# Kernel optimization log

Measured on AMD Instinct MI355X. Metric: run time of the kernel, lower is better.

Reference implementation:

```python
import jax, jax.numpy as jnp
import numpy as np

NH, NKV, D = 16, 8, 128
HID = 2048
EPS = 1e-6
ROPE_BASE = 10000.0
T = 2048


def setup_inputs() -> dict:
    key = jax.random.key(0)
    k1, k2, k3 = jax.random.split(key, 3)
    return {
        "positions": jnp.arange(T, dtype=jnp.int32),
        "hidden_states": jax.random.normal(k1, (T, HID), dtype=jnp.float32),
        "w_qkv": jax.random.normal(k2, (HID, (NH + 2 * NKV) * D), dtype=jnp.float32) * 0.02,
        "w_o": jax.random.normal(k3, (NH * D, HID), dtype=jnp.float32) * 0.02,
        "q_norm_w": jnp.ones((D,), dtype=jnp.float32),
        "k_norm_w": jnp.ones((D,), dtype=jnp.float32),
    }


def _rmsnorm(x, w):
    # per-head RMSNorm over last dim (head_dim)
    return x * jax.lax.rsqrt(jnp.mean(x * x, axis=-1, keepdims=True) + EPS) * w


def reference(positions, hidden_states, w_qkv, w_o, q_norm_w, k_norm_w):
    t = hidden_states.shape[0]
    scale = D ** -0.5

    # fused QKV projection, then split
    qkv = hidden_states @ w_qkv                       # [T, (NH+2*NKV)*D]
    q, k, v = jnp.split(qkv, [NH * D, (NH + NKV) * D], axis=-1)
    q = q.reshape(t, NH, D)
    k = k.reshape(t, NKV, D)
    v = v.reshape(t, NKV, D)

    # per-head QK RMSNorm (Qwen3)
    q = _rmsnorm(q, q_norm_w)
    k = _rmsnorm(k, k_norm_w)

    # RoPE (neox style: rotate half-split pairs)
    inv_freq = 1.0 / (ROPE_BASE ** (jnp.arange(0, D, 2, dtype=jnp.float32) / D))
    freqs = positions.astype(jnp.float32)[:, None] * inv_freq  # [T, D/2]
    cos = jnp.cos(freqs)[:, None, :]                   # [T, 1, D/2]
    sin = jnp.sin(freqs)[:, None, :]

    def rope(x):
        x1, x2 = jnp.split(x, 2, axis=-1)
        return jnp.concatenate([x1 * cos - x2 * sin, x2 * cos + x1 * sin], axis=-1)

    q = rope(q)
    k = rope(k)

    # GQA: repeat kv heads
    g = NH // NKV
    kr = jnp.repeat(k, g, axis=1)                      # [T, NH, D]
    vr = jnp.repeat(v, g, axis=1)

    # causal attention
    scores = jnp.einsum('thd,shd->hts', q, kr) * scale  # [NH, T, T]
    causal = jnp.tril(jnp.ones((t, t), dtype=bool))
    scores = jnp.where(causal[None], scores, -jnp.inf)
    probs = jax.nn.softmax(scores, axis=-1)
    o = jnp.einsum('hts,shd->thd', probs, vr).reshape(t, NH * D)

    return o @ w_o
```

## Files before the change

### kernel.cpp

```cpp
#include <hip/hip_runtime.h>
#include <math.h>

#define T_TOK 2048
#define HIDDEN 2048
#define NH 16
#define NKV 8
#define DH 128

typedef unsigned short u16;
typedef __attribute__((ext_vector_type(8))) short bf16x8;
typedef __attribute__((ext_vector_type(4))) float f32x4;

__device__ __forceinline__ u16 f2bf(float f) {
  union { float f; unsigned u; } x; x.f = f;
  unsigned r = (x.u + 0x7fffu + ((x.u >> 16) & 1u)) >> 16;
  return (u16)r;
}

__device__ __forceinline__ float bf2f(u16 v) {
  union { unsigned u; float f; } x; x.u = ((unsigned)v) << 16;
  return x.f;
}

__device__ __forceinline__ void gload16(const void* g, void* l) {
  __builtin_amdgcn_global_load_lds((const __attribute__((address_space(1))) void*)g,
                                   (__attribute__((address_space(3))) void*)l,
                                   16, 0, 0);
}

__global__ __launch_bounds__(256) void prepass(const float* __restrict__ hidden,
                                               const float* __restrict__ w_qkv,
                                               const float* __restrict__ w_o,
                                               u16* __restrict__ Xb,
                                               u16* __restrict__ WqkvT,
                                               u16* __restrict__ WoT) {
  __shared__ float tile[64][65];
  const int b = blockIdx.x;
  if (b < 4096) {
    int i = b * 256 + threadIdx.x;
    float4 v = ((const float4*)hidden)[i];
    ushort4 o;
    o.x = f2bf(v.x); o.y = f2bf(v.y); o.z = f2bf(v.z); o.w = f2bf(v.w);
    ((ushort4*)Xb)[i] = o;
    return;
  }
  const float* in; u16* out; int R, Cdim, c0, r0;
  if (b < 6144) {
    int bb = b - 4096;
    in = w_qkv; out = WqkvT; R = 2048; Cdim = 4096;
    c0 = (bb & 63) * 64; r0 = (bb >> 6) * 64;
  } else {
    int bb = b - 6144;
    in = w_o; out = WoT; R = 2048; Cdim = 2048;
    c0 = (bb & 31) * 64; r0 = (bb >> 5) * 64;
  }
  const int tx = threadIdx.x & 63, ty = threadIdx.x >> 6;
#pragma unroll
  for (int i = 0; i < 64; i += 4)
    tile[ty + i][tx] = in[(size_t)(r0 + ty + i) * Cdim + c0 + tx];
  __syncthreads();
#pragma unroll
  for (int i = 0; i < 64; i += 4)
    out[(size_t)(c0 + ty + i) * R + r0 + tx] = f2bf(tile[tx][ty + i]);
}

__global__ __launch_bounds__(256) void add_parts4(const u16* __restrict__ a,
                                                  const u16* __restrict__ b,
                                                  const u16* __restrict__ c,
                                                  const u16* __restrict__ d,
                                                  float* __restrict__ o, int n4) {
  int i = blockIdx.x * blockDim.x + threadIdx.x;
  if (i < n4) {
    ushort4 x = ((const ushort4*)a)[i], y = ((const ushort4*)b)[i];
    ushort4 u = ((const ushort4*)c)[i], v = ((const ushort4*)d)[i];
    float4 z;
    z.x = bf2f(x.x) + bf2f(y.x) + bf2f(u.x) + bf2f(v.x);
    z.y = bf2f(x.y) + bf2f(y.y) + bf2f(u.y) + bf2f(v.y);
    z.z = bf2f(x.z) + bf2f(y.z) + bf2f(u.z) + bf2f(v.z);
    z.w = bf2f(x.w) + bf2f(y.w) + bf2f(u.w) + bf2f(v.w);
    ((float4*)o)[i] = z;
  }
}

__global__ __launch_bounds__(256) void rope_vt(const u16* __restrict__ qkv0,
                                               const u16* __restrict__ qkv1,
                                               const int* __restrict__ pos,
                                               const float* __restrict__ qw,
                                               const float* __restrict__ kw,
                                               u16* __restrict__ Qg,
                                               u16* __restrict__ Kg,
                                               u16* __restrict__ Vt,
                                               unsigned* __restrict__ counter) {
  __shared__ float tile[64][65];
  const int b = blockIdx.x;
  if (b < 12288) {
    const int wave = threadIdx.x >> 6, j = threadIdx.x & 63;
    const int idx = b * 4 + wave;
    const int t = idx & 2047, slot = idx >> 11;
    const float QSC = 0.088388347648318447f * 1.4426950408889634f;
    const size_t base_i = (size_t)t * 4096 + slot * 128;
    float x1 = bf2f(qkv0[base_i + j]) + bf2f(qkv1[base_i + j]);
    float x2 = bf2f(qkv0[base_i + j + 64]) + bf2f(qkv1[base_i + j + 64]);
    float ss = x1 * x1 + x2 * x2;
#pragma unroll
    for (int m = 1; m < 64; m <<= 1) ss += __shfl_xor(ss, m);
    float r = rsqrtf(ss * (1.0f / 128.0f) + 1e-6f);
    const bool isq = slot < NH;
    const float* w = isq ? qw : kw;
    float xn1 = x1 * r * w[j], xn2 = x2 * r * w[j + 64];
    float fp = (float)pos[t];
    float inv_freq = exp2f(-(float)j * (13.287712379549449f / 64.0f));
    float ang = fp * inv_freq;
    float sn, cs;
    sincosf(ang, &sn, &cs);
    float o1 = xn1 * cs - xn2 * sn;
    float o2 = xn2 * cs + xn1 * sn;
    if (isq) {
      size_t base = ((size_t)slot * T_TOK + t) * DH;
      Qg[base + j] = f2bf(o1 * QSC); Qg[base + 64 + j] = f2bf(o2 * QSC);
    } else {
      size_t base = ((size_t)(slot - NH) * T_TOK + t) * DH;
      Kg[base + j] = f2bf(o1); Kg[base + 64 + j] = f2bf(o2);
    }
    return;
  }
  if (b == 12288 && threadIdx.x == 0) *counter = 0u;
  const int bb = b - 12288;
  const int h = bb & 7, rest = bb >> 3;
  const int t0 = (rest & 31) * 64, d0 = (rest >> 5) * 64;
  const int tx = threadIdx.x & 63, ty = threadIdx.x >> 6;
#pragma unroll
  for (int i = 0; i < 64; i += 4) {
    size_t gi = (size_t)(t0 + ty + i) * 4096 + (NH + NKV) * DH + h * DH + d0 + tx;
    tile[ty + i][tx] = bf2f(qkv0[gi]) + bf2f(qkv1[gi]);
  }
  __syncthreads();
#pragma unroll
  for (int i = 0; i < 64; i += 4)
    Vt[((size_t)h * DH + d0 + ty + i) * T_TOK + t0 + tx] = f2bf(tile[tx][ty + i]);
}

__global__ __launch_bounds__(256) void gemm_bf16(const u16* __restrict__ A,
                                                 const u16* __restrict__ Bt,
                                                 void* __restrict__ Cout,
                                                 int M, int N, int K, int lda, int ldb,
                                                 int obf16) {
  __shared__ u16 Alds[128 * 64];
  __shared__ u16 Blds[128 * 64];
  A += (size_t)blockIdx.z * K;
  Bt += (size_t)blockIdx.z * K;
  const int m0 = blockIdx.y * 128, n0 = blockIdx.x * 128;
  const int wave = threadIdx.x >> 6, lane = threadIdx.x & 63;
  const int l15 = lane & 15, quad = lane >> 4;
  const int wr = wave >> 1, wc = wave & 1;

  const f32x4 zero = {0.f, 0.f, 0.f, 0.f};
  f32x4 acc[4][4];
#pragma unroll
  for (int i = 0; i < 4; ++i)
#pragma unroll
    for (int j = 0; j < 4; ++j) acc[i][j] = zero;

  for (int k0 = 0; k0 < K; k0 += 64) {
    __syncthreads();
#pragma unroll
    for (int c = 0; c < 4; ++c) {
      int chunk = wave * 4 + c;
      int slot = chunk * 64 + lane;
      int row = slot >> 3;
      int g = (slot & 7) ^ (row & 7);
      gload16(A + (size_t)(m0 + row) * lda + k0 + g * 8, &Alds[chunk * 512]);
      gload16(Bt + (size_t)(n0 + row) * ldb + k0 + g * 8, &Blds[chunk * 512]);
    }
    __syncthreads();
#pragma unroll
    for (int ksub = 0; ksub < 2; ++ksub) {
      bf16x8 af[4], bfr[4];
#pragma unroll
      for (int mt = 0; mt < 4; ++mt) {
        int r = wr * 64 + mt * 16 + l15;
        af[mt] = *(const bf16x8*)&Alds[r * 64 + (((ksub * 4 + quad) ^ (r & 7)) * 8)];
      }
#pragma unroll
      for (int nt = 0; nt < 4; ++nt) {
        int r = wc * 64 + nt * 16 + l15;
        bfr[nt] = *(const bf16x8*)&Blds[r * 64 + (((ksub * 4 + quad) ^ (r & 7)) * 8)];
      }
#pragma unroll
      for (int mt = 0; mt < 4; ++mt)
#pragma unroll
        for (int nt = 0; nt < 4; ++nt)
          acc[mt][nt] = __builtin_amdgcn_mfma_f32_16x16x32_bf16(af[mt], bfr[nt], acc[mt][nt], 0, 0, 0);
    }
  }
  if (obf16) {
    u16* C = (u16*)Cout + (size_t)blockIdx.z * M * N;
#pragma unroll
    for (int mt = 0; mt < 4; ++mt)
#pragma unroll
      for (int nt = 0; nt < 4; ++nt)
#pragma unroll
        for (int r = 0; r < 4; ++r)
          C[(size_t)(m0 + wr * 64 + mt * 16 + quad * 4 + r) * N + n0 + wc * 64 + nt * 16 + l15] =
              f2bf(acc[mt][nt][r]);
  } else {
    float* C = (float*)Cout + (size_t)blockIdx.z * M * N;
#pragma unroll
    for (int mt = 0; mt < 4; ++mt)
#pragma unroll
      for (int nt = 0; nt < 4; ++nt)
#pragma unroll
        for (int r = 0; r < 4; ++r)
          C[(size_t)(m0 + wr * 64 + mt * 16 + quad * 4 + r) * N + n0 + wc * 64 + nt * 16 + l15] =
              acc[mt][nt][r];
  }
}

__global__ __launch_bounds__(256) void attn_kernel(const u16* __restrict__ Qg,
                                                   const u16* __restrict__ Kg,
                                                   const u16* __restrict__ Vtg,
                                                   float* __restrict__ Opart,
                                                   float* __restrict__ Lpart,
                                                   unsigned* __restrict__ counter) {
  __shared__ u16 Klds[64 * 128];
  __shared__ u16 Vlds[128 * 64];
  __shared__ u16 Plds[4][16 * 72];
  __shared__ unsigned item_s;
  const int wave = threadIdx.x >> 6, lane = threadIdx.x & 63;
  const int l15 = lane & 15, quad = lane >> 4;
  u16* Pw = &Plds[wave][0];
  const f32x4 zero = {0.f, 0.f, 0.f, 0.f};
  const float4 zero4 = {0.f, 0.f, 0.f, 0.f};

  for (;;) {
    __syncthreads();
    if (threadIdx.x == 0) item_s = atomicAdd(counter, 1u);
    __syncthreads();
    const unsigned item = item_s;
    if (item >= 1024u) break;
    const int qt = 31 - (int)(item >> 5);
    const int s  = (int)(item >> 4) & 1;
    const int h  = (int)item & 15;
    const int kvh = h >> 1;
    const int slot = (h * 32 + qt) * 2 + s;
    const int j0 = s ? (qt + 2) >> 1 : 0;
    const int j1 = s ? qt + 1 : (qt + 2) >> 1;

    float* Oslot = Opart + (size_t)slot * (64 * 128);

    if (j0 >= j1) {
      for (int t = threadIdx.x; t < 64 * 128 / 4; t += 256) ((float4*)Oslot)[t] = zero4;
      if (threadIdx.x < 64) Lpart[slot * 64 + threadIdx.x] = 0.f;
      continue;
    }

    const u16* Qh = Qg + (size_t)h * T_TOK * DH;
    const u16* Kh = Kg + (size_t)kvh * T_TOK * DH;
    const u16* Vh = Vtg + (size_t)kvh * DH * T_TOK;
    const int qrow0 = qt * 64 + wave * 16;

    bf16x8 qf[4];
#pragma unroll
    for (int ks = 0; ks < 4; ++ks)
      qf[ks] = *(const bf16x8*)(Qh + (size_t)(qrow0 + l15) * DH + ks * 32 + quad * 8);

    f32x4 oacc[8];
#pragma unroll
    for (int i = 0; i < 8; ++i) oacc[i] = zero;
    float l_i[4] = {0.f, 0.f, 0.f, 0.f};

    for (int j = j0; j < j1; ++j) {
      __syncthreads();
#pragma unroll
      for (int c = 0; c < 4; ++c) {
        int chunk = wave * 4 + c;
        int sl = chunk * 64 + lane;
        {
          int ss = sl >> 4;
          int g = (sl & 15) ^ (ss & 15);
          gload16(Kh + ((size_t)(j * 64 + ss)) * DH + g * 8, &Klds[chunk * 512]);
        }
        {
          int d = sl >> 3;
          int g = (sl & 7) ^ (d & 7);
          gload16(Vh + (size_t)d * T_TOK + j * 64 + g * 8, &Vlds[chunk * 512]);
        }
      }
      __syncthreads();

      f32x4 sacc[4];
#pragma unroll
      for (int nt = 0; nt < 4; ++nt) sacc[nt] = zero;
#pragma unroll
      for (int nt = 0; nt < 4; ++nt) {
        int sr = nt * 16 + l15;
#pragma unroll
        for (int ks = 0; ks < 4; ++ks) {
          bf16x8 kf = *(const bf16x8*)&Klds[sr * 128 + (((ks * 4 + quad) ^ (sr & 15)) * 8)];
          sacc[nt] = __builtin_amdgcn_mfma_f32_16x16x32_bf16(qf[ks], kf, sacc[nt], 0, 0, 0);
        }
      }

      if (j == qt) {
#pragma unroll
        for (int nt = 0; nt < 4; ++nt)
#pragma unroll
          for (int r = 0; r < 4; ++r) {
            int col = j * 64 + nt * 16 + l15;
            int row = qrow0 + quad * 4 + r;
            if (col > row) sacc[nt][r] = -INFINITY;
          }
      }

#pragma unroll
      for (int nt = 0; nt < 4; ++nt)
#pragma unroll
        for (int r = 0; r < 4; ++r) {
          float pv = exp2f(sacc[nt][r]);
          unsigned u = __float_as_uint(pv);
          Pw[(quad * 4 + r) * 72 + nt * 16 + l15] = (u16)(u >> 16);
          l_i[r] += __uint_as_float(u & 0xffff0000u);
        }

      bf16x8 pf[2];
#pragma unroll
      for (int ks = 0; ks < 2; ++ks)
        pf[ks] = *(const bf16x8*)&Pw[l15 * 72 + ks * 32 + quad * 8];
#pragma unroll
      for (int ot = 0; ot < 8; ++ot) {
        int d = ot * 16 + l15;
#pragma unroll
        for (int ks = 0; ks < 2; ++ks) {
          bf16x8 vf = *(const bf16x8*)&Vlds[d * 64 + (((ks * 4 + quad) ^ (d & 7)) * 8)];
          oacc[ot] = __builtin_amdgcn_mfma_f32_16x16x32_bf16(pf[ks], vf, oacc[ot], 0, 0, 0);
        }
      }
    }

#pragma unroll
    for (int ot = 0; ot < 8; ++ot)
#pragma unroll
      for (int r = 0; r < 4; ++r)
        Oslot[(wave * 16 + quad * 4 + r) * 128 + ot * 16 + l15] = oacc[ot][r];
#pragma unroll
    for (int msk = 1; msk < 16; msk <<= 1)
#pragma unroll
      for (int r = 0; r < 4; ++r) l_i[r] += __shfl_xor(l_i[r], msk);
    if (l15 == 0) {
#pragma unroll
      for (int r = 0; r < 4; ++r)
        Lpart[slot * 64 + wave * 16 + quad * 4 + r] = l_i[r];
    }
  }
}

__global__ __launch_bounds__(256) void attn_merge(const float* __restrict__ Opart,
                                                  const float* __restrict__ Lpart,
                                                  u16* __restrict__ Og) {
  const int b = blockIdx.x;
  const int h = b & 15, qt = b >> 4;
  const int slot0 = (h * 32 + qt) * 2, slot1 = slot0 + 1;
  const float4* O0 = (const float4*)(Opart + (size_t)slot0 * (64 * 128));
  const float4* O1 = (const float4*)(Opart + (size_t)slot1 * (64 * 128));
#pragma unroll
  for (int it = 0; it < 8; ++it) {
    int idx = it * 256 + threadIdx.x;
    int r = idx >> 5, c4 = idx & 31;
    float rl = 1.0f / (Lpart[slot0 * 64 + r] + Lpart[slot1 * 64 + r]);
    float4 a = O0[idx], c = O1[idx];
    int row = qt * 64 + r, col = c4 * 4;
    u16* dst = Og + (size_t)row * (NH * DH) + h * DH + col;
    dst[0] = f2bf((a.x + c.x) * rl);
    dst[1] = f2bf((a.y + c.y) * rl);
    dst[2] = f2bf((a.z + c.z) * rl);
    dst[3] = f2bf((a.w + c.w) * rl);
  }
}

extern "C" void kernel_launch(void* const* d_in, const int* in_sizes, int n_in,
                              void* d_out, int out_size, void* d_ws, size_t ws_size,
                              hipStream_t stream) {
  (void)in_sizes; (void)n_in; (void)out_size; (void)ws_size;
  const int* positions = (const int*)d_in[0];
  const float* hidden  = (const float*)d_in[1];
  const float* w_qkv   = (const float*)d_in[2];
  const float* w_o     = (const float*)d_in[3];
  const float* q_norm  = (const float*)d_in[4];
  const float* k_norm  = (const float*)d_in[5];
  float* out = (float*)d_out;

  char* ws = (char*)d_ws;
  u16*   Xb    = (u16*)(ws);
  u16*   WqkvT = (u16*)(ws + ( 8ull << 20));
  u16*   WoT   = (u16*)(ws + (24ull << 20));
  u16*   P0    = (u16*)(ws + (32ull << 20));
  u16*   P1    = P0 + (size_t)T_TOK * 4096;
  u16*   Qg    = (u16*)(ws + (64ull << 20));
  u16*   Kg    = (u16*)(ws + (72ull << 20));
  u16*   Vt    = (u16*)(ws + (76ull << 20));
  u16*   AttnO = (u16*)(ws + (80ull << 20));
  float* Opart = (float*)(ws + (32ull << 20));
  float* Lpart = (float*)(ws);
  unsigned* ctr = (unsigned*)(ws + (512ull << 10));
  u16*   G2P   = (u16*)(ws + (32ull << 20));

  prepass<<<dim3(7168), 256, 0, stream>>>(hidden, w_qkv, w_o, Xb, WqkvT, WoT);

  gemm_bf16<<<dim3(4096 / 128, T_TOK / 128, 2), 256, 0, stream>>>(
      Xb, WqkvT, P0, T_TOK, 4096, 1024, HIDDEN, HIDDEN, 1);

  rope_vt<<<dim3(12288 + 512), 256, 0, stream>>>(P0, P1, positions,
                                                 q_norm, k_norm, Qg, Kg, Vt, ctr);

  attn_kernel<<<dim3(768), 256, 0, stream>>>(Qg, Kg, Vt, Opart, Lpart, ctr);
  attn_merge<<<dim3(512), 256, 0, stream>>>(Opart, Lpart, AttnO);

  gemm_bf16<<<dim3(HIDDEN / 128, T_TOK / 128, 4), 256, 0, stream>>>(
      AttnO, WoT, G2P, T_TOK, HIDDEN, 512, NH * DH, NH * DH, 1);
  const int n4 = T_TOK * HIDDEN / 4;
  add_parts4<<<dim3(n4 / 256), 256, 0, stream>>>(
      G2P, G2P + (size_t)T_TOK * HIDDEN, G2P + 2 * (size_t)T_TOK * HIDDEN,
      G2P + 3 * (size_t)T_TOK * HIDDEN, out, n4);
}
```

Baseline: 259.1 us.

## Replace GEMM with 256x256-tile, 4-stage pipelined kernel and XCD-aware block swizzle

Replaces the 128x128 single-buffered bf16 GEMM with a 256x256 tile kernel using 8 waves, a 4-deep LDS ring buffer of K=32 slices, and explicit vmcnt waits so global loads overlap MFMA work. Block indices are remapped across the 8 XCDs to improve L2 locality, and MFMA sections raise wave priority. This targets the barrier stalls and low reuse of the old GEMM. In exchange it uses 128KB of LDS per block, adds register pressure from 32 accumulators, and leaves only 256 blocks per launch, which may underfill the GPU.

```diff
diff --git a/kernel.cpp b/kernel.cpp
--- a/kernel.cpp
+++ b/kernel.cpp
@@ -140,78 +140,112 @@
     Vt[((size_t)h * DH + d0 + ty + i) * T_TOK + t0 + tx] = f2bf(tile[tx][ty + i]);
 }
 
-__global__ __launch_bounds__(256) void gemm_bf16(const u16* __restrict__ A,
-                                                 const u16* __restrict__ Bt,
-                                                 void* __restrict__ Cout,
-                                                 int M, int N, int K, int lda, int ldb,
-                                                 int obf16) {
-  __shared__ u16 Alds[128 * 64];
-  __shared__ u16 Blds[128 * 64];
-  A += (size_t)blockIdx.z * K;
-  Bt += (size_t)blockIdx.z * K;
-  const int m0 = blockIdx.y * 128, n0 = blockIdx.x * 128;
-  const int wave = threadIdx.x >> 6, lane = threadIdx.x & 63;
+__global__ __launch_bounds__(512, 2) void gemm256(const u16* __restrict__ A,
+                                                  const u16* __restrict__ Bt,
+                                                  void* __restrict__ Cout,
+                                                  int M, int N, int K, int lda, int ldb,
+                                                  int obf16) {
+  __shared__ __attribute__((aligned(128))) char lds[131072];
+
+  const int nx = N >> 8, ny = M >> 8;
+  const int flat = blockIdx.x;
+  const int per = gridDim.x >> 3;
+  const int swz = (flat & 7) * per + (flat >> 3);
+  const int by = swz % ny;
+  const int rest = swz / ny;
+  const int bx = rest % nx;
+  const int bz = rest / nx;
+  const int m0 = by << 8, n0 = bx << 8;
+  A += (size_t)bz * K;
+  Bt += (size_t)bz * K;
+
+  const int tid = threadIdx.x;
+  const int wave = tid >> 6, lane = tid & 63;
   const int l15 = lane & 15, quad = lane >> 4;
-  const int wr = wave >> 1, wc = wave & 1;
+  const int wr = wave >> 2, wc = wave & 3;
+
+  size_t aoff[2], boff[2];
+#pragma unroll
+  for (int c = 0; c < 2; ++c) {
+    int chunk = c * 512 + tid;
+    int line = chunk >> 3;
+    int ls8 = (chunk & 7) ^ (line & 7);
+    int row = line * 2 + (ls8 >> 2);
+    int ks = ls8 & 3;
+    aoff[c] = (size_t)(m0 + row) * lda + ks * 8;
+    boff[c] = (size_t)(n0 + row) * ldb + ks * 8;
+  }
+
+#define STAGE(tt) do {                                                  \
+    char* db = lds + ((tt) & 3) * 16384 + wave * 1024;                  \
+    const int kk = (tt) * 32;                                           \
+    gload16(A + aoff[0] + kk, db);                                      \
+    gload16(A + aoff[1] + kk, db + 8192);                               \
+    gload16(Bt + boff[0] + kk, db + 65536);                             \
+    gload16(Bt + boff[1] + kk, db + 65536 + 8192);                      \
+  } while (0)
+
+  const int fragoff = (l15 >> 1) * 128 +
+                      (((((l15 & 1) << 2) | quad) ^ ((l15 >> 1) & 7)) << 4);
 
   const f32x4 zero = {0.f, 0.f, 0.f, 0.f};
-  f32x4 acc[4][4];
-#pragma unroll
-  for (int i = 0; i < 4; ++i)
+  f32x4 acc[8][4];
+#pragma unroll
+  for (int i = 0; i < 8; ++i)
 #pragma unroll
     for (int j = 0; j < 4; ++j) acc[i][j] = zero;
 
-  for (int k0 = 0; k0 < K; k0 += 64) {
-    __syncthreads();
-#pragma unroll
-    for (int c = 0; c < 4; ++c) {
-      int chunk = wave * 4 + c;
-      int slot = chunk * 64 + lane;
-      int row = slot >> 3;
-      int g = (slot & 7) ^ (row & 7);
-      gload16(A + (size_t)(m0 + row) * lda + k0 + g * 8, &Alds[chunk * 512]);
-      gload16(Bt + (size_t)(n0 + row) * ldb + k0 + g * 8, &Blds[chunk * 512]);
-    }
-    __syncthreads();
-#pragma unroll
-    for (int ksub = 0; ksub < 2; ++ksub) {
-      bf16x8 af[4], bfr[4];
-#pragma unroll
-      for (int mt = 0; mt < 4; ++mt) {
-        int r = wr * 64 + mt * 16 + l15;
-        af[mt] = *(const bf16x8*)&Alds[r * 64 + (((ksub * 4 + quad) ^ (r & 7)) * 8)];
-      }
-#pragma unroll
-      for (int nt = 0; nt < 4; ++nt) {
-        int r = wc * 64 + nt * 16 + l15;
-        bfr[nt] = *(const bf16x8*)&Blds[r * 64 + (((ksub * 4 + quad) ^ (r & 7)) * 8)];
-      }
-#pragma unroll
-      for (int mt = 0; mt < 4; ++mt)
-#pragma unroll
-        for (int nt = 0; nt < 4; ++nt)
-          acc[mt][nt] = __builtin_amdgcn_mfma_f32_16x16x32_bf16(af[mt], bfr[nt], acc[mt][nt], 0, 0, 0);
-    }
-  }
+  const int NT = K >> 5;
+  STAGE(0); STAGE(1); STAGE(2);
+  asm volatile("s_waitcnt vmcnt(8)" ::: "memory");
+  __builtin_amdgcn_s_barrier();
+
+  for (int t = 0; t < NT; ++t) {
+    const char* As = lds + (t & 3) * 16384 + wr * 8192 + fragoff;
+    const char* Bs = lds + 65536 + (t & 3) * 16384 + wc * 4096 + fragoff;
+    bf16x8 af[8], bfr[4];
+#pragma unroll
+    for (int mt = 0; mt < 8; ++mt) af[mt] = *(const bf16x8*)(As + mt * 1024);
+#pragma unroll
+    for (int nt = 0; nt < 4; ++nt) bfr[nt] = *(const bf16x8*)(Bs + nt * 1024);
+
+    if (t + 3 < NT) STAGE(t + 3);
+
+    __builtin_amdgcn_s_setprio(1);
+#pragma unroll
+    for (int mt = 0; mt < 8; ++mt)
+#pragma unroll
+      for (int nt = 0; nt < 4; ++nt)
+        acc[mt][nt] = __builtin_amdgcn_mfma_f32_16x16x32_bf16(af[mt], bfr[nt], acc[mt][nt], 0, 0, 0);
+    __builtin_amdgcn_s_setprio(0);
+
+    const int rem = NT - 1 - t;
+    if (rem >= 3)      asm volatile("s_waitcnt vmcnt(8)" ::: "memory");
+    else if (rem == 2) asm volatile("s_waitcnt vmcnt(4)" ::: "memory");
+    else if (rem == 1) asm volatile("s_waitcnt vmcnt(0)" ::: "memory");
+    if (rem > 0) __builtin_amdgcn_s_barrier();
+  }
+#undef STAGE
+
   if (obf16) {
-    u16* C = (u16*)Cout + (size_t)blockIdx.z * M * N;
-#pragma unroll
-    for (int mt = 0; mt < 4; ++mt)
+    u16* C = (u16*)Cout + (size_t)bz * M * N;
+#pragma unroll
+    for (int mt = 0; mt < 8; ++mt)
 #pragma unroll
       for (int nt = 0; nt < 4; ++nt)
 #pragma unroll
         for (int r = 0; r < 4; ++r)
-          C[(size_t)(m0 + wr * 64 + mt * 16 + quad * 4 + r) * N + n0 + wc * 64 + nt * 16 + l15] =
+          C[(size_t)(m0 + wr * 128 + mt * 16 + quad * 4 + r) * N + n0 + wc * 64 + nt * 16 + l15] =
               f2bf(acc[mt][nt][r]);
   } else {
-    float* C = (float*)Cout + (size_t)blockIdx.z * M * N;
-#pragma unroll
-    for (int mt = 0; mt < 4; ++mt)
+    float* C = (float*)Cout + (size_t)bz * M * N;
+#pragma unroll
+    for (int mt = 0; mt < 8; ++mt)
 #pragma unroll
       for (int nt = 0; nt < 4; ++nt)
 #pragma unroll
         for (int r = 0; r < 4; ++r)
-          C[(size_t)(m0 + wr * 64 + mt * 16 + quad * 4 + r) * N + n0 + wc * 64 + nt * 16 + l15] =
+          C[(size_t)(m0 + wr * 128 + mt * 16 + quad * 4 + r) * N + n0 + wc * 64 + nt * 16 + l15] =
               acc[mt][nt][r];
   }
 }
@@ -406,7 +440,7 @@
 
   prepass<<<dim3(7168), 256, 0, stream>>>(hidden, w_qkv, w_o, Xb, WqkvT, WoT);
 
-  gemm_bf16<<<dim3(4096 / 128, T_TOK / 128, 2), 256, 0, stream>>>(
+  gemm256<<<dim3(256), 512, 0, stream>>>(
       Xb, WqkvT, P0, T_TOK, 4096, 1024, HIDDEN, HIDDEN, 1);
 
   rope_vt<<<dim3(12288 + 512), 256, 0, stream>>>(P0, P1, positions,
@@ -415,7 +449,7 @@
   attn_kernel<<<dim3(768), 256, 0, stream>>>(Qg, Kg, Vt, Opart, Lpart, ctr);
   attn_merge<<<dim3(512), 256, 0, stream>>>(Opart, Lpart, AttnO);
 
-  gemm_bf16<<<dim3(HIDDEN / 128, T_TOK / 128, 4), 256, 0, stream>>>(
+  gemm256<<<dim3(256), 512, 0, stream>>>(
       AttnO, WoT, G2P, T_TOK, HIDDEN, 512, NH * DH, NH * DH, 1);
   const int n4 = T_TOK * HIDDEN / 4;
   add_parts4<<<dim3(n4 / 256), 256, 0, stream>>>(
```

Result: faster. 251.8 us (-2.8%).
